# Kernel tuning notes

Hardware: AMD Instinct MI355X
Metric: run time of the kernel (lower is better)

Reference implementation:

```python
import jax, jax.numpy as jnp
import numpy as np

N_NODES = 100000
N_EDGES = 1000000
N_GRAPHS = 64
NODE_IN = 4
HID = 64
SIG = 16
NEG_SLOPE = 0.2


def _gat_layer(x, src, dst, W, a_src, a_dst, bias, n_nodes, concat):
    # W: [H*D, F_in], a_src/a_dst: [H, D], bias: [H*D] or [D]
    H, D = a_src.shape
    h = (x @ W.T).reshape(-1, H, D)                      # [N, H, D]
    alpha_src = jnp.sum(h * a_src[None], axis=-1)        # [N, H]
    alpha_dst = jnp.sum(h * a_dst[None], axis=-1)        # [N, H]
    e = alpha_src[src] + alpha_dst[dst]                  # [E, H]
    e = jax.nn.leaky_relu(e, NEG_SLOPE)
    # segment softmax over edges grouped by destination node
    e_max = jax.ops.segment_max(e, dst, num_segments=n_nodes)   # [N, H]
    e_exp = jnp.exp(e - e_max[dst])                              # [E, H]
    denom = jax.ops.segment_sum(e_exp, dst, num_segments=n_nodes)
    alpha = e_exp / denom[dst]                                   # [E, H]
    out = jax.ops.segment_sum(alpha[:, :, None] * h[src], dst, num_segments=n_nodes)  # [N,H,D]
    if concat:
        out = out.reshape(-1, H * D)
    else:
        out = out.mean(axis=1)
    return out + bias


def setup_inputs() -> dict:
    key = jax.random.key(0)
    ks = jax.random.split(key, 16)
    x = jax.random.normal(ks[0], (N_NODES, NODE_IN), dtype=jnp.float32)
    edge_index = jax.random.randint(ks[1], (2, N_EDGES), 0, N_NODES, dtype=jnp.int32)
    batch = jnp.sort(jax.random.randint(ks[2], (N_NODES,), 0, N_GRAPHS, dtype=jnp.int32))
    s = 0.1
    # conv1: heads=2, concat -> out 128
    w1 = jax.random.normal(ks[3], (2 * HID, NODE_IN), dtype=jnp.float32) * s
    att_src1 = jax.random.normal(ks[4], (2, HID), dtype=jnp.float32) * s
    att_dst1 = jax.random.normal(ks[5], (2, HID), dtype=jnp.float32) * s
    b1 = jnp.zeros((2 * HID,), dtype=jnp.float32)
    # conv2: heads=1, mean -> out 64
    w2 = jax.random.normal(ks[6], (HID, 2 * HID), dtype=jnp.float32) * s
    att_src2 = jax.random.normal(ks[7], (1, HID), dtype=jnp.float32) * s
    att_dst2 = jax.random.normal(ks[8], (1, HID), dtype=jnp.float32) * s
    b2 = jnp.zeros((HID,), dtype=jnp.float32)
    wp = jax.random.normal(ks[9], (SIG, HID), dtype=jnp.float32) * s
    bp = jnp.zeros((SIG,), dtype=jnp.float32)
    return {"x": x, "edge_index": edge_index, "batch": batch,
            "w1": w1, "att_src1": att_src1, "att_dst1": att_dst1, "b1": b1,
            "w2": w2, "att_src2": att_src2, "att_dst2": att_dst2, "b2": b2,
            "wp": wp, "bp": bp}


def reference(x, edge_index, batch, w1, att_src1, att_dst1, b1,
              w2, att_src2, att_dst2, b2, wp, bp):
    n = x.shape[0]
    loops = jnp.arange(n, dtype=edge_index.dtype)
    src = jnp.concatenate([edge_index[0], loops])  # PyG GATConv adds self-loops
    dst = jnp.concatenate([edge_index[1], loops])
    h = jax.nn.elu(_gat_layer(x, src, dst, w1, att_src1, att_dst1, b1, n, concat=True))
    h = jax.nn.elu(_gat_layer(h, src, dst, w2, att_src2, att_dst2, b2, n, concat=False))
    # global mean pool by graph id
    sums = jax.ops.segment_sum(h, batch, num_segments=N_GRAPHS)
    cnts = jax.ops.segment_sum(jnp.ones((n,), h.dtype), batch, num_segments=N_GRAPHS)
    pooled = sums / jnp.maximum(cnts, 1.0)[:, None]
    return (pooled @ wp.T + bp).squeeze()
```

## Files before the change

kernel.cpp:

```cpp
#include <hip/hip_runtime.h>
#include <hip/hip_fp16.h>

#define N_NODES  100000
#define N_EDGES  1000000
#define E_TOT    1100000
#define E_CAP    1900000
#define N_GRAPHS 64

#define BSH    9
#define BSIZE  512
#define NBUCK  ((N_NODES + BSIZE - 1) / BSIZE)
#define CHUNK  4096
#define NBLKS  ((E_TOT + CHUNK - 1) / CHUNK)

typedef _Float16 half8 __attribute__((ext_vector_type(8)));
typedef float    f32x4 __attribute__((ext_vector_type(4)));

__device__ __forceinline__ float elu_f(float v) {
    return v > 0.f ? v : expm1f(v);
}

__device__ __forceinline__ float lrelu(float v) {
    return v > 0.f ? v : 0.2f * v;
}

__global__ void k_preall(const float* __restrict__ w1,
                         const float* __restrict__ as1v, const float* __restrict__ ad1v,
                         const float* __restrict__ w2,
                         const float* __restrict__ as2v, const float* __restrict__ ad2v,
                         float* __restrict__ A1, float* __restrict__ D1,
                         float* __restrict__ B2, float* __restrict__ E2,
                         __half* __restrict__ w2frag,
                         int* __restrict__ bucketCount, float* __restrict__ poolcnt)
{
    if (blockIdx.x == 0) {
        int t = threadIdx.x;
        if (t < 128) {
            float acc = 0.f;
            for (int d = 0; d < 64; ++d) acc += w2[d * 128 + t] * as2v[d];
            B2[t] = acc;
        } else {
            int k = t - 128;
            float acc = 0.f;
            for (int d = 0; d < 64; ++d) acc += w2[d * 128 + k] * ad2v[d];
            E2[k] = acc;
        }
        if (t < 8) {
            int h = t >> 2, k = t & 3;
            float acc = 0.f;
            for (int d = 0; d < 64; ++d) acc += w1[(h * 64 + d) * 4 + k] * as1v[h * 64 + d];
            A1[t] = acc;
        } else if (t < 16) {
            int i = t - 8, h = i >> 2, k = i & 3;
            float acc = 0.f;
            for (int d = 0; d < 64; ++d) acc += w1[(h * 64 + d) * 4 + k] * ad1v[h * 64 + d];
            D1[i] = acc;
        }
        if (t < NBUCK) bucketCount[t] = 0;
    } else {
        int f = (blockIdx.x - 1) * 256 + threadIdx.x;
        int j = f & 7, ln = (f >> 3) & 63, g = f >> 9;
        int nt = g >> 2, ks = g & 3;
        int col = nt * 16 + (ln & 15);
        int k   = ks * 32 + ((ln >> 4) << 3) + j;
        w2frag[f] = __float2half(w2[col * 128 + k]);
        int z = (blockIdx.x - 1) * 256 + threadIdx.x;
        if (z < N_GRAPHS * 64 + N_GRAPHS) poolcnt[z] = 0.f;
    }
}

__global__ void __launch_bounds__(256) k_bin1(
    const int* __restrict__ ei, int* __restrict__ bucketCount, int* __restrict__ blockoff)
{
    __shared__ int hist[NBUCK];
    const int t = threadIdx.x;
    for (int i = t; i < NBUCK; i += 256) hist[i] = 0;
    __syncthreads();
    const int e0 = blockIdx.x * CHUNK;
    for (int i = t; i < CHUNK; i += 256) {
        int e = e0 + i;
        if (e < E_TOT) {
            int dst = (e < N_EDGES) ? ei[N_EDGES + e] : (e - N_EDGES);
            atomicAdd(&hist[dst >> BSH], 1);
        }
    }
    __syncthreads();
    for (int i = t; i < NBUCK; i += 256)
        blockoff[blockIdx.x * NBUCK + i] = atomicAdd(&bucketCount[i], hist[i]);
}

__global__ void k_bscan(const int* __restrict__ bucketCount, int* __restrict__ bucketStart)
{
    __shared__ int sh[256];
    int t = threadIdx.x;
    int v = (t < NBUCK) ? bucketCount[t] : 0;
    int acc = v;
    sh[t] = acc; __syncthreads();
    for (int off = 1; off < 256; off <<= 1) {
        int add = (t >= off) ? sh[t - off] : 0;
        __syncthreads();
        acc += add; sh[t] = acc; __syncthreads();
    }
    if (t < NBUCK) bucketStart[t] = acc - v;
}

__global__ void __launch_bounds__(256) k_bin2(
    const int* __restrict__ ei, const int* __restrict__ bucketStart,
    const int* __restrict__ blockoff, unsigned int* __restrict__ bucketed)
{
    __shared__ int cur[NBUCK];
    const int t = threadIdx.x;
    for (int i = t; i < NBUCK; i += 256)
        cur[i] = bucketStart[i] + blockoff[blockIdx.x * NBUCK + i];
    __syncthreads();
    const int e0 = blockIdx.x * CHUNK;
    for (int i = t; i < CHUNK; i += 256) {
        int e = e0 + i;
        if (e < E_TOT) {
            int src = (e < N_EDGES) ? ei[e] : (e - N_EDGES);
            int dst = (e < N_EDGES) ? ei[N_EDGES + e] : (e - N_EDGES);
            int b = dst >> BSH;
            int p = atomicAdd(&cur[b], 1);
            bucketed[p] = (unsigned)src | ((unsigned)(dst & (BSIZE - 1)) << 17);
        }
    }
}

__global__ void __launch_bounds__(256) k_bhist(
    const unsigned int* __restrict__ bucketed,
    const int* __restrict__ bucketStart, const int* __restrict__ bucketCount,
    int* __restrict__ deg, int* __restrict__ rowptr, int* __restrict__ bucketPad)
{
    __shared__ int hist[BSIZE];
    __shared__ int sh[256];
    const int t = threadIdx.x;
    const int b = blockIdx.x;
    hist[t] = 0; hist[t + 256] = 0;
    __syncthreads();
    const int beg = bucketStart[b], cnt = bucketCount[b];
    for (int i = t; i < cnt; i += 256)
        atomicAdd(&hist[bucketed[beg + i] >> 17], 1);
    __syncthreads();
    int h0 = hist[2 * t], h1 = hist[2 * t + 1];
    int a = (h0 + 7) & ~7, c = (h1 + 7) & ~7;
    int s = a + c;
    sh[t] = s; __syncthreads();
    for (int off = 1; off < 256; off <<= 1) {
        int add = (t >= off) ? sh[t - off] : 0;
        __syncthreads();
        s += add; sh[t] = s; __syncthreads();
    }
    int base = s - a - c;
    const int n0 = b * BSIZE;
    int na = n0 + 2 * t, nb = n0 + 2 * t + 1;
    if (na < N_NODES) { deg[na] = h0; rowptr[na] = base; }
    if (nb < N_NODES) { deg[nb] = h1; rowptr[nb] = base + a; }
    if (t == 255) bucketPad[b] = s;
}

__global__ void k_bscan2(const int* __restrict__ bucketPad, int* __restrict__ bucketBase,
                         int* __restrict__ rowptr)
{
    __shared__ int sh[256];
    int t = threadIdx.x;
    int v = (t < NBUCK) ? bucketPad[t] : 0;
    int acc = v;
    sh[t] = acc; __syncthreads();
    for (int off = 1; off < 256; off <<= 1) {
        int add = (t >= off) ? sh[t - off] : 0;
        __syncthreads();
        acc += add; sh[t] = acc; __syncthreads();
    }
    if (t < NBUCK) bucketBase[t] = acc - v;
    if (t == NBUCK - 1) rowptr[N_NODES] = acc;
}

__global__ void __launch_bounds__(256) k_bscat(
    const unsigned int* __restrict__ bucketed,
    const int* __restrict__ bucketStart, const int* __restrict__ bucketCount,
    const int* __restrict__ bucketBase, const int* __restrict__ bucketPad,
    int* __restrict__ rowptr, int* __restrict__ srcs)
{
    __shared__ int cur[BSIZE];
    const int t = threadIdx.x;
    const int b = blockIdx.x;
    const int base = bucketBase[b];
    const int n0 = b * BSIZE;
    #pragma unroll
    for (int k = 0; k < 2; ++k) {
        int nl = t + k * 256;
        int n = n0 + nl;
        if (n < N_NODES) {
            int r = rowptr[n] + base;
            rowptr[n] = r;
            cur[nl] = r;
        }
    }
    __syncthreads();
    const int beg = bucketStart[b], cnt = bucketCount[b];
    for (int i = t; i < cnt; i += 256) {
        unsigned p = bucketed[beg + i];
        int rank = atomicAdd(&cur[p >> 17], 1);
        srcs[rank] = (int)(p & 0x1FFFFu);
    }
    __syncthreads();
    const int bend = base + bucketPad[b];
    #pragma unroll
    for (int k = 0; k < 2; ++k) {
        int nl = t + k * 256;
        int n = n0 + nl;
        if (n < N_NODES) {
            int e = (nl == BSIZE - 1 || n == N_NODES - 1) ? bend : rowptr[n + 1];
            for (int j = cur[nl]; j < e; ++j) srcs[j] = -1;
        }
    }
}

__global__ void __launch_bounds__(256) k_gather1x(
    const int* __restrict__ srcs, const int* __restrict__ rowptr, const int* __restrict__ deg,
    const float* __restrict__ x,
    const float* __restrict__ A1c, const float* __restrict__ D1c,
    float4* __restrict__ agg0, float4* __restrict__ agg1, float2* __restrict__ wsA)
{
    const int tid  = threadIdx.x;
    const int n    = blockIdx.x * 16 + (tid >> 4);
    const int lane = tid & 15;
    if (n >= N_NODES) return;

    const float4 A0 = ((const float4*)A1c)[0], A1v = ((const float4*)A1c)[1];
    const float4 D0 = ((const float4*)D1c)[0], D1v = ((const float4*)D1c)[1];
    const float4 xn = ((const float4*)x)[n];
    const float ad0 = xn.x * D0.x + xn.y * D0.y + xn.z * D0.z + xn.w * D0.w;
    const float ad1 = xn.x * D1v.x + xn.y * D1v.y + xn.z * D1v.z + xn.w * D1v.w;

    const int beg = rowptr[n], rend = beg + deg[n];
    float4 acc0 = {0.f, 0.f, 0.f, 0.f}, acc1 = {0.f, 0.f, 0.f, 0.f};
    float ws0 = 0.f, ws1 = 0.f;
    for (int j = beg + lane; j < rend; j += 16) {
        const int s = srcs[j];
        const float4 xs = ((const float4*)x)[s];
        const float as0 = xs.x * A0.x + xs.y * A0.y + xs.z * A0.z + xs.w * A0.w;
        const float as1 = xs.x * A1v.x + xs.y * A1v.y + xs.z * A1v.z + xs.w * A1v.w;
        const float w0 = __expf(lrelu(as0 + ad0));
        const float w1 = __expf(lrelu(as1 + ad1));
        acc0.x = fmaf(w0, xs.x, acc0.x); acc0.y = fmaf(w0, xs.y, acc0.y);
        acc0.z = fmaf(w0, xs.z, acc0.z); acc0.w = fmaf(w0, xs.w, acc0.w);
        acc1.x = fmaf(w1, xs.x, acc1.x); acc1.y = fmaf(w1, xs.y, acc1.y);
        acc1.z = fmaf(w1, xs.z, acc1.z); acc1.w = fmaf(w1, xs.w, acc1.w);
        ws0 += w0; ws1 += w1;
    }
    #pragma unroll
    for (int off = 1; off < 16; off <<= 1) {
        acc0.x += __shfl_xor(acc0.x, off, 64);
        acc0.y += __shfl_xor(acc0.y, off, 64);
        acc0.z += __shfl_xor(acc0.z, off, 64);
        acc0.w += __shfl_xor(acc0.w, off, 64);
        acc1.x += __shfl_xor(acc1.x, off, 64);
        acc1.y += __shfl_xor(acc1.y, off, 64);
        acc1.z += __shfl_xor(acc1.z, off, 64);
        acc1.w += __shfl_xor(acc1.w, off, 64);
        ws0    += __shfl_xor(ws0,    off, 64);
        ws1    += __shfl_xor(ws1,    off, 64);
    }
    if (lane == 0) {
        agg0[n] = acc0;
        agg1[n] = acc1;
        wsA[n]  = make_float2(ws0, ws1);
    }
}

#define H2_NPB 64
#define SROW_H_LD 136
__global__ void __launch_bounds__(256) k_h2f(
    const float4* __restrict__ agg0, const float4* __restrict__ agg1,
    const float2* __restrict__ wsA,
    const float* __restrict__ w1, const float* __restrict__ b1,
    const __half* __restrict__ w2frag,
    const float* __restrict__ B2, const float* __restrict__ E2,
    __half* __restrict__ h2h, float* __restrict__ as2, float* __restrict__ ad2)
{
    __shared__ __align__(16) _Float16 srow[H2_NPB * SROW_H_LD];
    const int tid = threadIdx.x;
    const int bn  = blockIdx.x * H2_NPB;

    #pragma unroll 4
    for (int t = 0; t < 16; ++t) {
        int i = tid + t * 256;
        int r = i >> 6, c2 = i & 63;
        int n = bn + r;
        int head = c2 >> 5;
        float4 a; float ws;
        if (n < N_NODES) {
            a = head ? agg1[n] : agg0[n];
            float2 w = wsA[n];
            ws = head ? w.y : w.x;
        } else { a = make_float4(0.f, 0.f, 0.f, 0.f); ws = 1.f; }
        const float4 wA = ((const float4*)w1)[2 * c2];
        const float4 wB = ((const float4*)w1)[2 * c2 + 1];
        const float2 bb = ((const float2*)b1)[c2];
        float inv = 1.f / ws;
        float v0 = elu_f((a.x * wA.x + a.y * wA.y + a.z * wA.z + a.w * wA.w) * inv + bb.x);
        float v1 = elu_f((a.x * wB.x + a.y * wB.y + a.z * wB.z + a.w * wB.w) * inv + bb.y);
        *(__half2*)&srow[r * SROW_H_LD + 2 * c2] = __floats2half2_rn(v0, v1);
    }
    __syncthreads();

    {
        int r = tid >> 2, q = tid & 3;
        const __half2* row = (const __half2*)&srow[r * SROW_H_LD];
        float ps = 0.f, pd = 0.f;
        #pragma unroll 4
        for (int i = 0; i < 16; ++i) {
            int c2 = q * 16 + i;
            float2 v  = __half22float2(row[c2]);
            float2 Bv = ((const float2*)B2)[c2];
            float2 Ev = ((const float2*)E2)[c2];
            ps += v.x * Bv.x + v.y * Bv.y;
            pd += v.x * Ev.x + v.y * Ev.y;
        }
        ps += __shfl_xor(ps, 1, 64); ps += __shfl_xor(ps, 2, 64);
        pd += __shfl_xor(pd, 1, 64); pd += __shfl_xor(pd, 2, 64);
        int n = bn + r;
        if (q == 0 && n < N_NODES) { as2[n] = ps; ad2[n] = pd; }
    }

    const int lane = tid & 63;
    const int wv   = tid >> 6;
    const int mrow = lane & 15;
    const int kc   = lane >> 4;
    f32x4 acc[4] = {{0.f,0.f,0.f,0.f},{0.f,0.f,0.f,0.f},{0.f,0.f,0.f,0.f},{0.f,0.f,0.f,0.f}};
    const half8* __restrict__ wf = (const half8*)w2frag;
    #pragma unroll
    for (int ks = 0; ks < 4; ++ks) {
        const half8 af = *(const half8*)&srow[(wv * 16 + mrow) * SROW_H_LD + ks * 32 + kc * 8];
        #pragma unroll
        for (int nt = 0; nt < 4; ++nt) {
            const half8 bf = wf[(nt * 4 + ks) * 64 + lane];
            acc[nt] = __builtin_amdgcn_mfma_f32_16x16x32_f16(af, bf, acc[nt], 0, 0, 0);
        }
    }
    #pragma unroll
    for (int nt = 0; nt < 4; ++nt) {
        #pragma unroll
        for (int reg = 0; reg < 4; ++reg) {
            int node = bn + wv * 16 + ((lane >> 4) << 2) + reg;
            int dim  = nt * 16 + (lane & 15);
            if (node < N_NODES) h2h[(size_t)node * 64 + dim] = __float2half(acc[nt][reg]);
        }
    }
}

__global__ void __launch_bounds__(256) k_gather2(
    const int* __restrict__ srcs, const int* __restrict__ rowptr,
    const float* __restrict__ as2, const float* __restrict__ ad2,
    const _Float16* __restrict__ h2h, const float* __restrict__ b2,
    float* __restrict__ out2)
{
    const int tid  = threadIdx.x;
    const int n    = blockIdx.x * 4 + (tid >> 6);
    const int lane = tid & 63;
    const int eg   = lane >> 3;
    const int dq   = lane & 7;
    const int beg = rowptr[n], end = rowptr[n + 1];
    const float adv = ad2[n];

    half8 hacc = {0, 0, 0, 0, 0, 0, 0, 0};
    float wsum = 0.f;
    for (int j = beg + eg; j < end; j += 8) {
        const int s = srcs[j];
        const int sa = (s >= 0) ? s : 0;
        float w = 0.f;
        if (s >= 0) w = __expf(lrelu(as2[s] + adv));
        const half8 v = *(const half8*)&h2h[(size_t)sa * 64 + dq * 8];
        const _Float16 wh = (_Float16)w;
        const half8 ws8 = {wh, wh, wh, wh, wh, wh, wh, wh};
        hacc += v * ws8;
        wsum += w;
    }
    float a0 = (float)hacc[0], a1 = (float)hacc[1], a2 = (float)hacc[2], a3 = (float)hacc[3];
    float a4 = (float)hacc[4], a5 = (float)hacc[5], a6 = (float)hacc[6], a7 = (float)hacc[7];
    #pragma unroll
    for (int off = 8; off < 64; off <<= 1) {
        a0 += __shfl_xor(a0, off, 64);
        a1 += __shfl_xor(a1, off, 64);
        a2 += __shfl_xor(a2, off, 64);
        a3 += __shfl_xor(a3, off, 64);
        a4 += __shfl_xor(a4, off, 64);
        a5 += __shfl_xor(a5, off, 64);
        a6 += __shfl_xor(a6, off, 64);
        a7 += __shfl_xor(a7, off, 64);
        wsum += __shfl_xor(wsum, off, 64);
    }
    if (eg == 0) {
        const float inv = 1.f / wsum;
        const float4 bA = ((const float4*)b2)[dq * 2];
        const float4 bB = ((const float4*)b2)[dq * 2 + 1];
        float4 oA, oB;
        oA.x = elu_f(a0 * inv + bA.x);
        oA.y = elu_f(a1 * inv + bA.y);
        oA.z = elu_f(a2 * inv + bA.z);
        oA.w = elu_f(a3 * inv + bA.w);
        oB.x = elu_f(a4 * inv + bB.x);
        oB.y = elu_f(a5 * inv + bB.y);
        oB.z = elu_f(a6 * inv + bB.z);
        oB.w = elu_f(a7 * inv + bB.w);
        float4* orow = (float4*)(out2 + (size_t)n * 64);
        orow[dq * 2]     = oA;
        orow[dq * 2 + 1] = oB;
    }
}

__global__ void __launch_bounds__(256) k_pool(
    const float* __restrict__ out2, const int* __restrict__ batch,
    float* __restrict__ pool, float* __restrict__ cnt)
{
    const int wv = threadIdx.x >> 6, d = threadIdx.x & 63;
    const int wid = blockIdx.x * 4 + wv;
    const int per = (N_NODES + 2047) / 2048;
    int n0 = wid * per, n1 = min(n0 + per, N_NODES);
    if (n0 >= n1) return;
    float acc = 0.f; int g = batch[n0]; int run = 0;
    for (int n = n0; n < n1; ++n) {
        int gn = batch[n];
        if (gn != g) {
            atomicAdd(&pool[g * 64 + d], acc);
            if (d == 0) atomicAdd(&cnt[g], (float)run);
            acc = 0.f; run = 0; g = gn;
        }
        acc += out2[(size_t)n * 64 + d];
        ++run;
    }
    atomicAdd(&pool[g * 64 + d], acc);
    if (d == 0) atomicAdd(&cnt[g], (float)run);
}

__global__ void k_head(const float* __restrict__ pool, const float* __restrict__ cnt,
                       const float* __restrict__ wp, const float* __restrict__ bp,
                       float* __restrict__ out)
{
    int t = threadIdx.x;
    int g = t >> 4, s = t & 15;
    float c = cnt[g]; if (c < 1.f) c = 1.f;
    float acc = bp[s];
    for (int d = 0; d < 64; ++d) acc += (pool[g * 64 + d] / c) * wp[s * 64 + d];
    out[g * 16 + s] = acc;
}

extern "C" void kernel_launch(void* const* d_in, const int* in_sizes, int n_in,
                              void* d_out, int out_size, void* d_ws, size_t ws_size,
                              hipStream_t stream)
{
    const float* x     = (const float*)d_in[0];
    const int*   ei    = (const int*)  d_in[1];
    const int*   batch = (const int*)  d_in[2];
    const float* w1    = (const float*)d_in[3];
    const float* asr1  = (const float*)d_in[4];
    const float* adr1  = (const float*)d_in[5];
    const float* b1    = (const float*)d_in[6];
    const float* w2    = (const float*)d_in[7];
    const float* asr2  = (const float*)d_in[8];
    const float* adr2  = (const float*)d_in[9];
    const float* b2    = (const float*)d_in[10];
    const float* wp    = (const float*)d_in[11];
    const float* bp    = (const float*)d_in[12];
    float* out = (float*)d_out;

    float4* agg0 = (float4*)d_ws;
    float4* agg1 = agg0 + N_NODES;
    float2* wsA  = (float2*)(agg1 + N_NODES);
    __half* h2h  = (__half*)(wsA + N_NODES);
    float* out2  = (float*)(h2h + (size_t)N_NODES * 64);
    float* as2   = out2 + (size_t)N_NODES * 64;
    float* ad2   = as2 + N_NODES;
    float* pool  = ad2 + N_NODES;
    float* cnt   = pool + N_GRAPHS * 64;
    int* deg     = (int*)(cnt + N_GRAPHS);
    int* rowptr  = deg + N_NODES;
    unsigned int* bucketed = (unsigned int*)(rowptr + N_NODES + 1);
    int* srcs    = (int*)(bucketed + E_TOT);
    int* blockoff    = srcs + E_CAP;
    int* bucketCount = blockoff + NBLKS * NBUCK;
    int* bucketStart = bucketCount + NBUCK;
    int* bucketPad   = bucketStart + NBUCK;
    int* bucketBase  = bucketPad + NBUCK;
    float* A1    = (float*)(bucketBase + NBUCK);
    float* D1    = A1 + 8;
    float* B2    = D1 + 8;
    float* E2    = B2 + 128;
    __half* w2frag = (__half*)(((uintptr_t)(E2 + 128) + 15) & ~(uintptr_t)15);

    k_preall<<<33, 256, 0, stream>>>(w1, asr1, adr1, w2, asr2, adr2,
                                     A1, D1, B2, E2, w2frag, bucketCount, pool);

    k_bin1 <<<NBLKS, 256, 0, stream>>>(ei, bucketCount, blockoff);
    k_bscan<<<1, 256, 0, stream>>>(bucketCount, bucketStart);
    k_bin2 <<<NBLKS, 256, 0, stream>>>(ei, bucketStart, blockoff, bucketed);
    k_bhist<<<NBUCK, 256, 0, stream>>>(bucketed, bucketStart, bucketCount, deg, rowptr, bucketPad);
    k_bscan2<<<1, 256, 0, stream>>>(bucketPad, bucketBase, rowptr);
    k_bscat<<<NBUCK, 256, 0, stream>>>(bucketed, bucketStart, bucketCount, bucketBase,
                                       bucketPad, rowptr, srcs);

    const int gb = (N_NODES + 15) / 16;
    k_gather1x<<<gb, 256, 0, stream>>>(srcs, rowptr, deg, x, A1, D1, agg0, agg1, wsA);

    k_h2f<<<(N_NODES + H2_NPB - 1) / H2_NPB, 256, 0, stream>>>(
        agg0, agg1, wsA, w1, b1, w2frag, B2, E2, h2h, as2, ad2);

    k_gather2<<<N_NODES / 4, 256, 0, stream>>>(srcs, rowptr, as2, ad2,
                                               (const _Float16*)h2h, b2, out2);

    k_pool<<<512, 256, 0, stream>>>(out2, batch, pool, cnt);
    k_head<<<1, 1024, 0, stream>>>(pool, cnt, wp, bp, out);
}
```

Baseline: 197.5 us.

## Fold scan kernels into consumers, store layer-2 output as fp16, precompute graph counts

The two single-block scan kernels are removed: each block of k_bin2 and k_bscat now recomputes the small bucket prefix scan in shared memory, which drops two launches and their serialization points. The layer-2 output is written as fp16 instead of fp32, halving the write in gather2 and the read in k_pool. Per-graph node counts are computed once by binary search on the sorted batch array in k_preall, replacing atomics in k_pool. The costs are redundant scan work in every block and reduced precision of the pooled activations.

Measured after the change: 195.6 us. Within noise of the previous version (-1.0%).

```diff
diff --git a/kernel.cpp b/kernel.cpp
--- a/kernel.cpp
+++ b/kernel.cpp
@@ -22,6 +22,12 @@
 
 __device__ __forceinline__ float lrelu(float v) {
     return v > 0.f ? v : 0.2f * v;
+}
+
+__device__ __forceinline__ int lbound(const int* __restrict__ a, int n, int v) {
+    int lo = 0, hi = n;
+    while (lo < hi) { int m = (lo + hi) >> 1; if (a[m] < v) lo = m + 1; else hi = m; }
+    return lo;
 }
 
 __global__ void k_preall(const float* __restrict__ w1,
@@ -31,7 +37,8 @@
                          float* __restrict__ A1, float* __restrict__ D1,
                          float* __restrict__ B2, float* __restrict__ E2,
                          __half* __restrict__ w2frag,
-                         int* __restrict__ bucketCount, float* __restrict__ poolcnt)
+                         int* __restrict__ bucketCount, float* __restrict__ pool,
+                         const int* __restrict__ batch, float* __restrict__ cnt)
 {
     if (blockIdx.x == 0) {
         int t = threadIdx.x;
@@ -57,6 +64,11 @@
             D1[i] = acc;
         }
         if (t < NBUCK) bucketCount[t] = 0;
+        if (t < N_GRAPHS) {
+            int a = lbound(batch, N_NODES, t);
+            int b = lbound(batch, N_NODES, t + 1);
+            cnt[t] = (float)(b - a);
+        }
     } else {
         int f = (blockIdx.x - 1) * 256 + threadIdx.x;
         int j = f & 7, ln = (f >> 3) & 63, g = f >> 9;
@@ -64,8 +76,7 @@
         int col = nt * 16 + (ln & 15);
         int k   = ks * 32 + ((ln >> 4) << 3) + j;
         w2frag[f] = __float2half(w2[col * 128 + k]);
-        int z = (blockIdx.x - 1) * 256 + threadIdx.x;
-        if (z < N_GRAPHS * 64 + N_GRAPHS) poolcnt[z] = 0.f;
+        if (f < N_GRAPHS * 64) pool[f] = 0.f;
     }
 }
 
@@ -89,10 +100,14 @@
         blockoff[blockIdx.x * NBUCK + i] = atomicAdd(&bucketCount[i], hist[i]);
 }
 
-__global__ void k_bscan(const int* __restrict__ bucketCount, int* __restrict__ bucketStart)
+__global__ void __launch_bounds__(256) k_bin2(
+    const int* __restrict__ ei, const int* __restrict__ bucketCount,
+    const int* __restrict__ blockoff, int* __restrict__ bucketStart,
+    unsigned int* __restrict__ bucketed)
 {
     __shared__ int sh[256];
-    int t = threadIdx.x;
+    __shared__ int cur[NBUCK];
+    const int t = threadIdx.x;
     int v = (t < NBUCK) ? bucketCount[t] : 0;
     int acc = v;
     sh[t] = acc; __syncthreads();
@@ -101,17 +116,11 @@
         __syncthreads();
         acc += add; sh[t] = acc; __syncthreads();
     }
-    if (t < NBUCK) bucketStart[t] = acc - v;
-}
-
-__global__ void __launch_bounds__(256) k_bin2(
-    const int* __restrict__ ei, const int* __restrict__ bucketStart,
-    const int* __restrict__ blockoff, unsigned int* __restrict__ bucketed)
-{
-    __shared__ int cur[NBUCK];
-    const int t = threadIdx.x;
-    for (int i = t; i < NBUCK; i += 256)
-        cur[i] = bucketStart[i] + blockoff[blockIdx.x * NBUCK + i];
+    if (t < NBUCK) {
+        int st = acc - v;
+        cur[t] = st + blockoff[blockIdx.x * NBUCK + t];
+        if (blockIdx.x == 0) bucketStart[t] = st;
+    }
     __syncthreads();
     const int e0 = blockIdx.x * CHUNK;
     for (int i = t; i < CHUNK; i += 256) {
@@ -158,11 +167,18 @@
     if (t == 255) bucketPad[b] = s;
 }
 
-__global__ void k_bscan2(const int* __restrict__ bucketPad, int* __restrict__ bucketBase,
-                         int* __restrict__ rowptr)
+__global__ void __launch_bounds__(256) k_bscat(
+    const unsigned int* __restrict__ bucketed,
+    const int* __restrict__ bucketStart, const int* __restrict__ bucketCount,
+    const int* __restrict__ bucketPad,
+    int* __restrict__ rowptr, int* __restrict__ srcs)
 {
     __shared__ int sh[256];
-    int t = threadIdx.x;
+    __shared__ int excl[NBUCK];
+    __shared__ int cur[BSIZE];
+    const int t = threadIdx.x;
+    const int b = blockIdx.x;
+
     int v = (t < NBUCK) ? bucketPad[t] : 0;
     int acc = v;
     sh[t] = acc; __syncthreads();
@@ -171,20 +187,11 @@
         __syncthreads();
         acc += add; sh[t] = acc; __syncthreads();
     }
-    if (t < NBUCK) bucketBase[t] = acc - v;
-    if (t == NBUCK - 1) rowptr[N_NODES] = acc;
-}
-
-__global__ void __launch_bounds__(256) k_bscat(
-    const unsigned int* __restrict__ bucketed,
-    const int* __restrict__ bucketStart, const int* __restrict__ bucketCount,
-    const int* __restrict__ bucketBase, const int* __restrict__ bucketPad,
-    int* __restrict__ rowptr, int* __restrict__ srcs)
-{
-    __shared__ int cur[BSIZE];
-    const int t = threadIdx.x;
-    const int b = blockIdx.x;
-    const int base = bucketBase[b];
+    if (t < NBUCK) excl[t] = acc - v;
+    if (b == 0 && t == NBUCK - 1) rowptr[N_NODES] = acc;
+    __syncthreads();
+    const int base = excl[b];
+
     const int n0 = b * BSIZE;
     #pragma unroll
     for (int k = 0; k < 2; ++k) {
@@ -354,7 +361,7 @@
     const int* __restrict__ srcs, const int* __restrict__ rowptr,
     const float* __restrict__ as2, const float* __restrict__ ad2,
     const _Float16* __restrict__ h2h, const float* __restrict__ b2,
-    float* __restrict__ out2)
+    __half* __restrict__ out2h)
 {
     const int tid  = threadIdx.x;
     const int n    = blockIdx.x * 4 + (tid >> 6);
@@ -395,43 +402,36 @@
         const float inv = 1.f / wsum;
         const float4 bA = ((const float4*)b2)[dq * 2];
         const float4 bB = ((const float4*)b2)[dq * 2 + 1];
-        float4 oA, oB;
-        oA.x = elu_f(a0 * inv + bA.x);
-        oA.y = elu_f(a1 * inv + bA.y);
-        oA.z = elu_f(a2 * inv + bA.z);
-        oA.w = elu_f(a3 * inv + bA.w);
-        oB.x = elu_f(a4 * inv + bB.x);
-        oB.y = elu_f(a5 * inv + bB.y);
-        oB.z = elu_f(a6 * inv + bB.z);
-        oB.w = elu_f(a7 * inv + bB.w);
-        float4* orow = (float4*)(out2 + (size_t)n * 64);
-        orow[dq * 2]     = oA;
-        orow[dq * 2 + 1] = oB;
+        __half2 p0 = __floats2half2_rn(elu_f(a0 * inv + bA.x), elu_f(a1 * inv + bA.y));
+        __half2 p1 = __floats2half2_rn(elu_f(a2 * inv + bA.z), elu_f(a3 * inv + bA.w));
+        __half2 p2 = __floats2half2_rn(elu_f(a4 * inv + bB.x), elu_f(a5 * inv + bB.y));
+        __half2 p3 = __floats2half2_rn(elu_f(a6 * inv + bB.z), elu_f(a7 * inv + bB.w));
+        uint4 pk;
+        pk.x = *(unsigned int*)&p0; pk.y = *(unsigned int*)&p1;
+        pk.z = *(unsigned int*)&p2; pk.w = *(unsigned int*)&p3;
+        *(uint4*)&out2h[(size_t)n * 64 + dq * 8] = pk;
     }
 }
 
 __global__ void __launch_bounds__(256) k_pool(
-    const float* __restrict__ out2, const int* __restrict__ batch,
-    float* __restrict__ pool, float* __restrict__ cnt)
+    const __half* __restrict__ out2h, const int* __restrict__ batch,
+    float* __restrict__ pool)
 {
     const int wv = threadIdx.x >> 6, d = threadIdx.x & 63;
     const int wid = blockIdx.x * 4 + wv;
     const int per = (N_NODES + 2047) / 2048;
     int n0 = wid * per, n1 = min(n0 + per, N_NODES);
     if (n0 >= n1) return;
-    float acc = 0.f; int g = batch[n0]; int run = 0;
+    float acc = 0.f; int g = batch[n0];
     for (int n = n0; n < n1; ++n) {
         int gn = batch[n];
         if (gn != g) {
             atomicAdd(&pool[g * 64 + d], acc);
-            if (d == 0) atomicAdd(&cnt[g], (float)run);
-            acc = 0.f; run = 0; g = gn;
-        }
-        acc += out2[(size_t)n * 64 + d];
-        ++run;
+            acc = 0.f; g = gn;
+        }
+        acc += __half2float(out2h[(size_t)n * 64 + d]);
     }
     atomicAdd(&pool[g * 64 + d], acc);
-    if (d == 0) atomicAdd(&cnt[g], (float)run);
 }
 
 __global__ void k_head(const float* __restrict__ pool, const float* __restrict__ cnt,
@@ -469,8 +469,8 @@
     float4* agg1 = agg0 + N_NODES;
     float2* wsA  = (float2*)(agg1 + N_NODES);
     __half* h2h  = (__half*)(wsA + N_NODES);
-    float* out2  = (float*)(h2h + (size_t)N_NODES * 64);
-    float* as2   = out2 + (size_t)N_NODES * 64;
+    __half* out2h = h2h + (size_t)N_NODES * 64;
+    float* as2   = (float*)(out2h + (size_t)N_NODES * 64);
     float* ad2   = as2 + N_NODES;
     float* pool  = ad2 + N_NODES;
     float* cnt   = pool + N_GRAPHS * 64;
@@ -482,23 +482,21 @@
     int* bucketCount = blockoff + NBLKS * NBUCK;
     int* bucketStart = bucketCount + NBUCK;
     int* bucketPad   = bucketStart + NBUCK;
-    int* bucketBase  = bucketPad + NBUCK;
-    float* A1    = (float*)(bucketBase + NBUCK);
+    float* A1    = (float*)(bucketPad + NBUCK);
     float* D1    = A1 + 8;
     float* B2    = D1 + 8;
     float* E2    = B2 + 128;
     __half* w2frag = (__half*)(((uintptr_t)(E2 + 128) + 15) & ~(uintptr_t)15);
 
     k_preall<<<33, 256, 0, stream>>>(w1, asr1, adr1, w2, asr2, adr2,
-                                     A1, D1, B2, E2, w2frag, bucketCount, pool);
+                                     A1, D1, B2, E2, w2frag, bucketCount, pool,
+                                     batch, cnt);
 
     k_bin1 <<<NBLKS, 256, 0, stream>>>(ei, bucketCount, blockoff);
-    k_bscan<<<1, 256, 0, stream>>>(bucketCount, bucketStart);
-    k_bin2 <<<NBLKS, 256, 0, stream>>>(ei, bucketStart, blockoff, bucketed);
+    k_bin2 <<<NBLKS, 256, 0, stream>>>(ei, bucketCount, blockoff, bucketStart, bucketed);
     k_bhist<<<NBUCK, 256, 0, stream>>>(bucketed, bucketStart, bucketCount, deg, rowptr, bucketPad);
-    k_bscan2<<<1, 256, 0, stream>>>(bucketPad, bucketBase, rowptr);
-    k_bscat<<<NBUCK, 256, 0, stream>>>(bucketed, bucketStart, bucketCount, bucketBase,
-                                       bucketPad, rowptr, srcs);
+    k_bscat<<<NBUCK, 256, 0, stream>>>(bucketed, bucketStart, bucketCount, bucketPad,
+                                       rowptr, srcs);
 
     const int gb = (N_NODES + 15) / 16;
     k_gather1x<<<gb, 256, 0, stream>>>(srcs, rowptr, deg, x, A1, D1, agg0, agg1, wsA);
@@ -507,8 +505,8 @@
         agg0, agg1, wsA, w1, b1, w2frag, B2, E2, h2h, as2, ad2);
 
     k_gather2<<<N_NODES / 4, 256, 0, stream>>>(srcs, rowptr, as2, ad2,
-                                               (const _Float16*)h2h, b2, out2);
-
-    k_pool<<<512, 256, 0, stream>>>(out2, batch, pool, cnt);
+                                               (const _Float16*)h2h, b2, out2h);
+
+    k_pool<<<512, 256, 0, stream>>>(out2h, batch, pool);
     k_head<<<1, 1024, 0, stream>>>(pool, cnt, wp, bp, out);
 }
```
